# Optimization experiments

Hardware: AMD Instinct MI355X
Metric: run time of the kernel (lower is better)

The kernel has to match this reference:

```python
import jax, jax.numpy as jnp
import numpy as np

N, E, D = 50000, 800000, 128
LN_EPS = 1e-5


def setup_inputs() -> dict:
    key = jax.random.key(0)
    ks = jax.random.split(key, 6)
    return {
        "x": jax.random.normal(ks[0], (N, D), dtype=jnp.float32),
        "edge_index": jax.random.randint(ks[1], (2, E), 0, N, dtype=jnp.int64),
        "edge_weight": jax.random.uniform(ks[2], (E,), dtype=jnp.float32),
        "lin_w": jax.random.normal(ks[3], (D, D), dtype=jnp.float32) * (1.0 / np.sqrt(D)),
        "lin_b": jax.random.normal(ks[4], (D,), dtype=jnp.float32) * 0.02,
        "ln_gamma": jnp.ones((D,), dtype=jnp.float32),
        "ln_beta": jnp.zeros((D,), dtype=jnp.float32),
    }


def reference(x, edge_index, edge_weight, lin_w, lin_b, ln_gamma, ln_beta):
    n = x.shape[0]
    src, dst = edge_index[0], edge_index[1]
    # degree (by dst), symmetric-ish normalization with +1 smoothing
    deg = jax.ops.segment_sum(jnp.ones(dst.shape, x.dtype), dst, num_segments=n)
    dis = jax.lax.rsqrt(deg + 1.0)  # (N,)
    # gather -> scale -> scatter-add
    scale = (edge_weight * dis[src])[:, None]          # (E,1)
    msg = x[src] * scale                               # (E,D)
    agg = jax.ops.segment_sum(msg, dst, num_segments=n)  # (N,D)
    agg = agg * dis[:, None] + x                       # residual
    # dense tail: Linear -> GELU (exact, matches torch F.gelu) -> LayerNorm
    h = jax.nn.gelu(agg @ lin_w.T + lin_b, approximate=False)
    mu = jnp.mean(h, axis=-1, keepdims=True)
    var = jnp.mean(jnp.square(h - mu), axis=-1, keepdims=True)
    return (h - mu) * jax.lax.rsqrt(var + LN_EPS) * ln_gamma + ln_beta
```

## Files before the change

kernel.cpp:

```cpp
#include <hip/hip_runtime.h>
#include <hip/hip_fp16.h>
#include <math.h>

#define D 128
#define CAP 48
#define LDS_STRIDE 136
#define CHUNKS 256
#define BLDS 4096

typedef __bf16  bf16x8 __attribute__((ext_vector_type(8)));
typedef float   f32x4  __attribute__((ext_vector_type(4)));

static __device__ __forceinline__ unsigned short f2bf(float f) {
    unsigned int u = __float_as_uint(f);
    u = (u + 0x7fffu + ((u >> 16) & 1u)) >> 16;
    return (unsigned short)u;
}
static __device__ __forceinline__ unsigned int pack2bf(float lo, float hi) {
    return (unsigned int)f2bf(lo) | ((unsigned int)f2bf(hi) << 16);
}
static __device__ __forceinline__ float bflo(unsigned int u) { return __uint_as_float(u << 16); }
static __device__ __forceinline__ float bfhi(unsigned int u) { return __uint_as_float(u & 0xffff0000u); }


__global__ __launch_bounds__(256) void k_hist(const int* __restrict__ dst,
                                              int* __restrict__ H,
                                              int e_count, int cs, int nbk) {
    __shared__ int hist[1024];
    int tid = threadIdx.x, c = blockIdx.x;
    for (int b = tid; b < nbk; b += 256) hist[b] = 0;
    __syncthreads();
    int lo = c * cs, hi = min(lo + cs, e_count);
    for (int i = lo + tid; i < hi; i += 256) atomicAdd(&hist[dst[i] >> 6], 1);
    __syncthreads();
    for (int b = tid; b < nbk; b += 256) H[b * CHUNKS + c] = hist[b];
}

__global__ __launch_bounds__(256) void k_bsum(const int* __restrict__ a,
                                              int* __restrict__ bsum, int n) {
    int g = blockIdx.x * 256 + threadIdx.x;
    int lane = threadIdx.x & 63, wave = threadIdx.x >> 6;
    int v = (g < n) ? a[g] : 0;
    #pragma unroll
    for (int off = 32; off > 0; off >>= 1) v += __shfl_down(v, off);
    __shared__ int ws[4];
    if (lane == 0) ws[wave] = v;
    __syncthreads();
    if (threadIdx.x == 0) bsum[blockIdx.x] = ws[0] + ws[1] + ws[2] + ws[3];
}

__global__ __launch_bounds__(1024) void k_scan_bsum2(int* __restrict__ bsum, int nb) {
    int tid = threadIdx.x, lane = tid & 63, wave = tid >> 6;
    int v = (tid < nb) ? bsum[tid] : 0;
    int incl = v;
    #pragma unroll
    for (int off = 1; off < 64; off <<= 1) {
        int t = __shfl_up(incl, off);
        if (lane >= off) incl += t;
    }
    __shared__ int ws[16];
    if (lane == 63) ws[wave] = incl;
    __syncthreads();
    if (tid == 0) {
        int run = 0;
        #pragma unroll
        for (int i = 0; i < 16; ++i) { int t = ws[i]; ws[i] = run; run += t; }
    }
    __syncthreads();
    if (tid < nb) bsum[tid] = incl - v + ws[wave];
}

__global__ __launch_bounds__(256) void k_applyH(int* __restrict__ H,
                                                const int* __restrict__ bsum_excl, int m) {
    int g = blockIdx.x * 256 + threadIdx.x;
    int tid = threadIdx.x, lane = tid & 63, wave = tid >> 6;
    int v = (g < m) ? H[g] : 0;
    int incl = v;
    #pragma unroll
    for (int off = 1; off < 64; off <<= 1) {
        int t = __shfl_up(incl, off);
        if (lane >= off) incl += t;
    }
    __shared__ int ws[4];
    if (lane == 63) ws[wave] = incl;
    __syncthreads();
    int add = bsum_excl[blockIdx.x];
    for (int i = 0; i < wave; ++i) add += ws[i];
    if (g < m) H[g] = incl - v + add;
}

__global__ __launch_bounds__(256) void k_scatter(const int* __restrict__ src,
                                                 const int* __restrict__ dst,
                                                 const float* __restrict__ ew,
                                                 const int* __restrict__ H,
                                                 unsigned int* __restrict__ rec,
                                                 int e_count, int cs, int nbk) {
    __shared__ int cur[1024];
    int tid = threadIdx.x, c = blockIdx.x;
    for (int b = tid; b < nbk; b += 256) cur[b] = H[b * CHUNKS + c];
    __syncthreads();
    int lo = c * cs, hi = min(lo + cs, e_count);
    for (int i = lo + tid; i < hi; i += 256) {
        int d = dst[i];
        int s = src[i];
        unsigned int q = (unsigned int)(ew[i] * 1023.0f + 0.5f);
        unsigned int r = (q << 22) | ((unsigned int)(d & 63) << 16) | (unsigned int)s;
        int pos = atomicAdd(&cur[d >> 6], 1);
        rec[pos] = r;
    }
}

__global__ __launch_bounds__(256) void k_bucket_sort(unsigned int* __restrict__ rec,
                                                     const int* __restrict__ H,
                                                     int* __restrict__ deg,
                                                     int* __restrict__ offs,
                                                     int e_count, int n, int nbk) {
    __shared__ int hist[64], curs[64];
    __shared__ unsigned int srt[BLDS];
    int tid = threadIdx.x, b = blockIdx.x;
    int start = H[b * CHUNKS];
    int end = (b == nbk - 1) ? e_count : H[(b + 1) * CHUNKS];
    int cnt = min(end - start, BLDS);
    if (tid < 64) hist[tid] = 0;
    __syncthreads();
    for (int i = tid; i < cnt; i += 256) atomicAdd(&hist[(rec[start + i] >> 16) & 63], 1);
    __syncthreads();
    if (tid < 64) {
        int dg = hist[tid];
        int incl = dg;
        #pragma unroll
        for (int off = 1; off < 64; off <<= 1) {
            int t = __shfl_up(incl, off);
            if (tid >= off) incl += t;
        }
        int excl = incl - dg;
        curs[tid] = excl;
        int node = b * 64 + tid;
        if (node < n) {
            deg[node] = dg;
            offs[node] = start + excl;
            if (node == n - 1) offs[n] = e_count;
        }
    }
    __syncthreads();
    for (int i = tid; i < cnt; i += 256) {
        unsigned int r = rec[start + i];
        int rank = atomicAdd(&curs[(r >> 16) & 63], 1);
        srt[rank] = r;
    }
    __syncthreads();
    for (int i = tid; i < cnt; i += 256) rec[start + i] = srt[i];
}


__global__ __launch_bounds__(256) void k_cast(const float* __restrict__ x,
                                              const int* __restrict__ deg,
                                              unsigned short* __restrict__ xs, int n) {
    int i4 = blockIdx.x * 256 + threadIdx.x;
    int nq = n * (D / 4);
    if (i4 >= nq) return;
    int node = i4 >> 5;
    float dd = rsqrtf((float)deg[node] + 1.0f);
    float4 v = ((const float4*)x)[i4];
    ushort4 u;
    u.x = f2bf(v.x * dd); u.y = f2bf(v.y * dd);
    u.z = f2bf(v.z * dd); u.w = f2bf(v.w * dd);
    ((ushort4*)xs)[i4] = u;
}


__global__ __launch_bounds__(256) void k_gather_csr(const unsigned short* __restrict__ xs,
                                                    const float* __restrict__ x,
                                                    const int* __restrict__ offs,
                                                    const unsigned int* __restrict__ rec,
                                                    unsigned short* __restrict__ aggbf, int n) {
    int node = (int)((blockIdx.x * blockDim.x + threadIdx.x) >> 6);
    int lane = threadIdx.x & 63;
    if (node >= n) return;
    int beg = offs[node], end = offs[node + 1];
    const float wq = 1.0f / 1023.0f;
    float ax = 0.f, ay = 0.f;

    int e = beg;
    for (; e + 3 < end; e += 4) {
        unsigned int r0 = rec[e + 0], r1 = rec[e + 1], r2 = rec[e + 2], r3 = rec[e + 3];
        unsigned int u0 = ((const unsigned int*)(xs + (size_t)(r0 & 0xffffu) * D))[lane];
        unsigned int u1 = ((const unsigned int*)(xs + (size_t)(r1 & 0xffffu) * D))[lane];
        unsigned int u2 = ((const unsigned int*)(xs + (size_t)(r2 & 0xffffu) * D))[lane];
        unsigned int u3 = ((const unsigned int*)(xs + (size_t)(r3 & 0xffffu) * D))[lane];
        float w0 = (float)(r0 >> 22) * wq;
        float w1 = (float)(r1 >> 22) * wq;
        float w2 = (float)(r2 >> 22) * wq;
        float w3 = (float)(r3 >> 22) * wq;
        ax += w0 * bflo(u0); ay += w0 * bfhi(u0);
        ax += w1 * bflo(u1); ay += w1 * bfhi(u1);
        ax += w2 * bflo(u2); ay += w2 * bfhi(u2);
        ax += w3 * bflo(u3); ay += w3 * bfhi(u3);
    }
    for (; e < end; ++e) {
        unsigned int r = rec[e];
        unsigned int u = ((const unsigned int*)(xs + (size_t)(r & 0xffffu) * D))[lane];
        float w = (float)(r >> 22) * wq;
        ax += w * bflo(u); ay += w * bfhi(u);
    }

    float dd = rsqrtf((float)(end - beg) + 1.0f);
    float2 xv = ((const float2*)(x + (size_t)node * D))[lane];
    ((unsigned int*)(aggbf + (size_t)node * D))[lane] = pack2bf(ax * dd + xv.x, ay * dd + xv.y);
}


__global__ __launch_bounds__(256) void k_tail_bf(const unsigned short* __restrict__ aggbf,
                                                 float* __restrict__ out,
                                                 const float* __restrict__ W,
                                                 const float* __restrict__ bias,
                                                 const float* __restrict__ gamma,
                                                 const float* __restrict__ beta, int n) {
    __shared__ unsigned short Bl[128 * LDS_STRIDE];

    int tid  = threadIdx.x;
    int lane = tid & 63;
    int wave = tid >> 6;
    int n16  = lane & 15;
    int quad = lane >> 4;

    #pragma unroll
    for (int it = 0; it < 16; ++it) {
        int idx4 = it * 256 + tid;
        float4 w4 = ((const float4*)W)[idx4];
        int t  = idx4 >> 5;
        int k4 = (idx4 & 31) << 2;
        ushort4 u;
        u.x = f2bf(w4.x); u.y = f2bf(w4.y); u.z = f2bf(w4.z); u.w = f2bf(w4.w);
        *(ushort4*)&Bl[t * LDS_STRIDE + k4] = u;
    }
    __syncthreads();

    int row0w = blockIdx.x * 64 + wave * 16;
    int arow  = row0w + n16;

    bf16x8 afr[4];
    #pragma unroll
    for (int ko = 0; ko < 4; ++ko)
        afr[ko] = __builtin_bit_cast(bf16x8,
            *(const uint4*)&aggbf[(size_t)arow * D + ko * 32 + quad * 8]);

    f32x4 acc[8];
    #pragma unroll
    for (int nt = 0; nt < 8; ++nt) acc[nt] = (f32x4){0.f, 0.f, 0.f, 0.f};

    #pragma unroll
    for (int nt = 0; nt < 8; ++nt) {
        #pragma unroll
        for (int ko = 0; ko < 4; ++ko) {
            bf16x8 bfr = __builtin_bit_cast(bf16x8,
                *(const uint4*)&Bl[(nt * 16 + n16) * LDS_STRIDE + ko * 32 + quad * 8]);
            acc[nt] = __builtin_amdgcn_mfma_f32_16x16x32_bf16(afr[ko], bfr, acc[nt], 0, 0, 0);
        }
    }

    float bcol[8], gcol[8], betcol[8];
    #pragma unroll
    for (int nt = 0; nt < 8; ++nt) {
        int col = nt * 16 + n16;
        bcol[nt]   = bias[col];
        gcol[nt]   = gamma[col];
        betcol[nt] = beta[col];
    }

    #pragma unroll
    for (int r = 0; r < 4; ++r) {
        float h[8];
        float s1 = 0.f, s2 = 0.f;
        #pragma unroll
        for (int nt = 0; nt < 8; ++nt) {
            float v = acc[nt][r] + bcol[nt];
            v = 0.5f * v * (1.0f + erff(v * 0.70710678118654752f));
            h[nt] = v;
            s1 += v; s2 += v * v;
        }
        #pragma unroll
        for (int mask = 1; mask < 16; mask <<= 1) {
            s1 += __shfl_xor(s1, mask);
            s2 += __shfl_xor(s2, mask);
        }
        float mu  = s1 * (1.0f / 128.0f);
        float var = s2 * (1.0f / 128.0f) - mu * mu;
        float inv = rsqrtf(var + 1e-5f);
        int row = row0w + quad * 4 + r;
        if (row < n) {
            #pragma unroll
            for (int nt = 0; nt < 8; ++nt)
                out[(size_t)row * D + nt * 16 + n16] = (h[nt] - mu) * inv * gcol[nt] + betcol[nt];
        }
    }
}


__global__ __launch_bounds__(256) void k_fillp8(const int* __restrict__ src,
                                                const int* __restrict__ dst,
                                                const float* __restrict__ ew,
                                                int* __restrict__ cnt,
                                                int2* __restrict__ rec, int e_count) {
    int e = blockIdx.x * blockDim.x + threadIdx.x;
    if (e >= e_count) return;
    int d = dst[e];
    int pos = atomicAdd(&cnt[d], 1);
    if (pos < CAP)
        rec[(size_t)d * CAP + pos] = make_int2(src[e], __float_as_int(ew[e]));
}

__global__ __launch_bounds__(256) void k_gatherp_f32(const float* __restrict__ x,
                                                     const int* __restrict__ cnt,
                                                     const int2* __restrict__ rec,
                                                     float* __restrict__ agg, int n) {
    int node = (int)((blockIdx.x * blockDim.x + threadIdx.x) >> 6);
    int lane = threadIdx.x & 63;
    if (node >= n) return;
    int c = cnt[node];
    int m = min(c, CAP);
    size_t base = (size_t)node * CAP;
    float ax = 0.f, ay = 0.f;
    for (int i = 0; i < m; ++i) {
        int2 p = rec[base + i];
        float w = __int_as_float(p.y) * rsqrtf((float)cnt[p.x] + 1.0f);
        float2 v = ((const float2*)(x + (size_t)p.x * D))[lane];
        ax += w * v.x; ay += w * v.y;
    }
    float dd = rsqrtf((float)c + 1.0f);
    float2 xv = ((const float2*)(x + (size_t)node * D))[lane];
    float2 o;
    o.x = ax * dd + xv.x;
    o.y = ay * dd + xv.y;
    ((float2*)(agg + (size_t)node * D))[lane] = o;
}

__global__ __launch_bounds__(256) void k_tail_mfma(float* __restrict__ io,
                                                   const float* __restrict__ W,
                                                   const float* __restrict__ bias,
                                                   const float* __restrict__ gamma,
                                                   const float* __restrict__ beta, int n) {
    __shared__ unsigned short Bl[128 * LDS_STRIDE];
    __shared__ unsigned short Al[4][16 * LDS_STRIDE];

    int tid  = threadIdx.x;
    int lane = tid & 63;
    int wave = tid >> 6;
    int n16  = lane & 15;
    int quad = lane >> 4;

    #pragma unroll
    for (int it = 0; it < 16; ++it) {
        int idx4 = it * 256 + tid;
        float4 w4 = ((const float4*)W)[idx4];
        int t  = idx4 >> 5;
        int k4 = (idx4 & 31) << 2;
        ushort4 u;
        u.x = f2bf(w4.x); u.y = f2bf(w4.y); u.z = f2bf(w4.z); u.w = f2bf(w4.w);
        *(ushort4*)&Bl[t * LDS_STRIDE + k4] = u;
    }
    int row0w = blockIdx.x * 64 + wave * 16;
    #pragma unroll
    for (int j = 0; j < 8; ++j) {
        int idx4 = j * 64 + lane;
        int m  = idx4 >> 5;
        int k4 = (idx4 & 31) << 2;
        int row = row0w + m;
        float4 a4 = make_float4(0.f, 0.f, 0.f, 0.f);
        if (row < n) a4 = ((const float4*)(io + (size_t)row * D))[idx4 & 31];
        ushort4 u;
        u.x = f2bf(a4.x); u.y = f2bf(a4.y); u.z = f2bf(a4.z); u.w = f2bf(a4.w);
        *(ushort4*)&Al[wave][m * LDS_STRIDE + k4] = u;
    }
    __syncthreads();

    bf16x8 afr[4];
    #pragma unroll
    for (int ko = 0; ko < 4; ++ko)
        afr[ko] = __builtin_bit_cast(bf16x8,
            *(const uint4*)&Al[wave][n16 * LDS_STRIDE + ko * 32 + quad * 8]);

    f32x4 acc[8];
    #pragma unroll
    for (int nt = 0; nt < 8; ++nt) acc[nt] = (f32x4){0.f, 0.f, 0.f, 0.f};

    #pragma unroll
    for (int nt = 0; nt < 8; ++nt) {
        #pragma unroll
        for (int ko = 0; ko < 4; ++ko) {
            bf16x8 bfr = __builtin_bit_cast(bf16x8,
                *(const uint4*)&Bl[(nt * 16 + n16) * LDS_STRIDE + ko * 32 + quad * 8]);
            acc[nt] = __builtin_amdgcn_mfma_f32_16x16x32_bf16(afr[ko], bfr, acc[nt], 0, 0, 0);
        }
    }

    float bcol[8], gcol[8], betcol[8];
    #pragma unroll
    for (int nt = 0; nt < 8; ++nt) {
        int col = nt * 16 + n16;
        bcol[nt]   = bias[col];
        gcol[nt]   = gamma[col];
        betcol[nt] = beta[col];
    }

    #pragma unroll
    for (int r = 0; r < 4; ++r) {
        float h[8];
        float s1 = 0.f, s2 = 0.f;
        #pragma unroll
        for (int nt = 0; nt < 8; ++nt) {
            float v = acc[nt][r] + bcol[nt];
            v = 0.5f * v * (1.0f + erff(v * 0.70710678118654752f));
            h[nt] = v;
            s1 += v; s2 += v * v;
        }
        #pragma unroll
        for (int mask = 1; mask < 16; mask <<= 1) {
            s1 += __shfl_xor(s1, mask);
            s2 += __shfl_xor(s2, mask);
        }
        float mu  = s1 * (1.0f / 128.0f);
        float var = s2 * (1.0f / 128.0f) - mu * mu;
        float inv = rsqrtf(var + 1e-5f);
        int row = row0w + quad * 4 + r;
        if (row < n) {
            #pragma unroll
            for (int nt = 0; nt < 8; ++nt)
                io[(size_t)row * D + nt * 16 + n16] = (h[nt] - mu) * inv * gcol[nt] + betcol[nt];
        }
    }
}


extern "C" void kernel_launch(void* const* d_in, const int* in_sizes, int n_in,
                              void* d_out, int out_size, void* d_ws, size_t ws_size,
                              hipStream_t stream) {
    const float* x    = (const float*)d_in[0];
    const int*   ei   = (const int*)d_in[1];
    const float* ew   = (const float*)d_in[2];
    const float* linw = (const float*)d_in[3];
    const float* linb = (const float*)d_in[4];
    const float* lng  = (const float*)d_in[5];
    const float* lnb  = (const float*)d_in[6];
    float* out = (float*)d_out;

    int n = in_sizes[0] / D;
    int e = in_sizes[1] / 2;
    const int* src = ei;
    const int* dst = ei + e;

    int nbk = (n + 63) / 64;
    int m   = nbk * CHUNKS;
    int cs  = (e + CHUNKS - 1) / CHUNKS;
    int gb  = (n + 3) / 4;
    int tb  = (n + 63) / 64;

    char* wsp = (char*)d_ws;
    size_t off = 0;
    auto alloc = [&](size_t bytes) { char* p = wsp + off; off = (off + bytes + 255) & ~(size_t)255; return p; };
    int*            H     = (int*)alloc((size_t)m * 4);
    int*            bsumH = (int*)alloc((size_t)nbk * 4);
    unsigned int*   rec   = (unsigned int*)alloc((size_t)e * 4);
    int*            deg   = (int*)alloc((size_t)n * 4);
    int*            offs  = (int*)alloc((size_t)(n + 1) * 4);
    unsigned short* xs    = (unsigned short*)alloc((size_t)n * D * 2);
    unsigned short* aggbf = (unsigned short*)alloc(((size_t)n + 64) * D * 2);
    bool big = (off <= ws_size) && (n <= 65535) && (nbk <= 1024);

    if (big) {
        k_hist<<<CHUNKS, 256, 0, stream>>>(dst, H, e, cs, nbk);
        k_bsum<<<nbk, 256, 0, stream>>>(H, bsumH, m);
        k_scan_bsum2<<<1, 1024, 0, stream>>>(bsumH, nbk);
        k_applyH<<<nbk, 256, 0, stream>>>(H, bsumH, m);
        k_scatter<<<CHUNKS, 256, 0, stream>>>(src, dst, ew, H, rec, e, cs, nbk);
        k_bucket_sort<<<nbk, 256, 0, stream>>>(rec, H, deg, offs, e, n, nbk);
        int cb = (n * (D / 4) + 255) / 256;
        k_cast<<<cb, 256, 0, stream>>>(x, deg, xs, n);
        k_gather_csr<<<gb, 256, 0, stream>>>(xs, x, offs, rec, aggbf, n);
        k_tail_bf<<<tb, 256, 0, stream>>>(aggbf, out, linw, linb, lng, lnb, n);
    } else {
        size_t off2 = 0;
        auto alloc2 = [&](size_t bytes) { char* p = wsp + off2; off2 = (off2 + bytes + 255) & ~(size_t)255; return p; };
        int*  cnt2 = (int*)alloc2((size_t)n * 4);
        int2* rec8 = (int2*)alloc2((size_t)n * CAP * 8);
        hipMemsetAsync(cnt2, 0, (size_t)n * 4, stream);
        int eb = (e + 255) / 256;
        k_fillp8<<<eb, 256, 0, stream>>>(src, dst, ew, cnt2, rec8, e);
        k_gatherp_f32<<<gb, 256, 0, stream>>>(x, cnt2, rec8, out, n);
        k_tail_mfma<<<tb, 256, 0, stream>>>(out, linw, linb, lng, lnb, n);
    }
}
```

Measured before the change: 175.3 us.

## Fuse bf16 cast into bucket sort and split gather into column slices

The separate cast kernel is folded into the bucket-sort kernel: each block scales and converts its own 64 node rows to bf16 using the degree histogram it already holds in LDS. This removes a launch and the deg array round-trip. The gather kernel is reworked so that each block handles one 32-column slice of four nodes. Within a wave, four lane groups process different edges in parallel and are reduced with shuffles. This raises the number of independent loads in flight per node, at the cost of four times as many blocks and re-reading the edge records once per slice.

```diff
diff --git a/kernel.cpp b/kernel.cpp
--- a/kernel.cpp
+++ b/kernel.cpp
@@ -110,11 +110,12 @@
     }
 }
 
-__global__ __launch_bounds__(256) void k_bucket_sort(unsigned int* __restrict__ rec,
-                                                     const int* __restrict__ H,
-                                                     int* __restrict__ deg,
-                                                     int* __restrict__ offs,
-                                                     int e_count, int n, int nbk) {
+__global__ __launch_bounds__(256) void k_bucket_sort_cast(unsigned int* __restrict__ rec,
+                                                          const int* __restrict__ H,
+                                                          const float* __restrict__ x,
+                                                          unsigned short* __restrict__ xs,
+                                                          int* __restrict__ offs,
+                                                          int e_count, int n, int nbk) {
     __shared__ int hist[64], curs[64];
     __shared__ unsigned int srt[BLDS];
     int tid = threadIdx.x, b = blockIdx.x;
@@ -137,12 +138,25 @@
         curs[tid] = excl;
         int node = b * 64 + tid;
         if (node < n) {
-            deg[node] = dg;
             offs[node] = start + excl;
             if (node == n - 1) offs[n] = e_count;
         }
     }
     __syncthreads();
+    #pragma unroll
+    for (int j = 0; j < 8; ++j) {
+        int idx = j * 256 + tid;
+        int rl = idx >> 5;
+        int node = b * 64 + rl;
+        if (node < n) {
+            float dd = rsqrtf((float)hist[rl] + 1.0f);
+            float4 v = ((const float4*)x)[(size_t)node * 32 + (idx & 31)];
+            ushort4 u;
+            u.x = f2bf(v.x * dd); u.y = f2bf(v.y * dd);
+            u.z = f2bf(v.z * dd); u.w = f2bf(v.w * dd);
+            ((ushort4*)xs)[(size_t)node * 32 + (idx & 31)] = u;
+        }
+    }
     for (int i = tid; i < cnt; i += 256) {
         unsigned int r = rec[start + i];
         int rank = atomicAdd(&curs[(r >> 16) & 63], 1);
@@ -153,60 +167,51 @@
 }
 
 
-__global__ __launch_bounds__(256) void k_cast(const float* __restrict__ x,
-                                              const int* __restrict__ deg,
-                                              unsigned short* __restrict__ xs, int n) {
-    int i4 = blockIdx.x * 256 + threadIdx.x;
-    int nq = n * (D / 4);
-    if (i4 >= nq) return;
-    int node = i4 >> 5;
-    float dd = rsqrtf((float)deg[node] + 1.0f);
-    float4 v = ((const float4*)x)[i4];
-    ushort4 u;
-    u.x = f2bf(v.x * dd); u.y = f2bf(v.y * dd);
-    u.z = f2bf(v.z * dd); u.w = f2bf(v.w * dd);
-    ((ushort4*)xs)[i4] = u;
-}
-
-
-__global__ __launch_bounds__(256) void k_gather_csr(const unsigned short* __restrict__ xs,
-                                                    const float* __restrict__ x,
-                                                    const int* __restrict__ offs,
-                                                    const unsigned int* __restrict__ rec,
-                                                    unsigned short* __restrict__ aggbf, int n) {
-    int node = (int)((blockIdx.x * blockDim.x + threadIdx.x) >> 6);
+__global__ __launch_bounds__(256) void k_gather_slice(const unsigned short* __restrict__ xs,
+                                                      const float* __restrict__ x,
+                                                      const int* __restrict__ offs,
+                                                      const unsigned int* __restrict__ rec,
+                                                      unsigned short* __restrict__ aggbf, int n) {
+    int slice = blockIdx.x & 3;
+    int wave  = threadIdx.x >> 6;
+    int node  = (blockIdx.x >> 2) * 4 + wave;
+    if (node >= n) return;
     int lane = threadIdx.x & 63;
-    if (node >= n) return;
+    int g    = lane >> 4;
+    int l    = lane & 15;
     int beg = offs[node], end = offs[node + 1];
+    int m = end - beg;
     const float wq = 1.0f / 1023.0f;
+    size_t soff = (size_t)slice * 32 + (size_t)l * 2;
+
     float ax = 0.f, ay = 0.f;
-
-    int e = beg;
-    for (; e + 3 < end; e += 4) {
-        unsigned int r0 = rec[e + 0], r1 = rec[e + 1], r2 = rec[e + 2], r3 = rec[e + 3];
-        unsigned int u0 = ((const unsigned int*)(xs + (size_t)(r0 & 0xffffu) * D))[lane];
-        unsigned int u1 = ((const unsigned int*)(xs + (size_t)(r1 & 0xffffu) * D))[lane];
-        unsigned int u2 = ((const unsigned int*)(xs + (size_t)(r2 & 0xffffu) * D))[lane];
-        unsigned int u3 = ((const unsigned int*)(xs + (size_t)(r3 & 0xffffu) * D))[lane];
+    int i = 0;
+    for (; i + 7 < m; i += 8) {
+        unsigned int r0 = rec[beg + i + g];
+        unsigned int r1 = rec[beg + i + 4 + g];
+        unsigned int u0 = *(const unsigned int*)(xs + (size_t)(r0 & 0xffffu) * D + soff);
+        unsigned int u1 = *(const unsigned int*)(xs + (size_t)(r1 & 0xffffu) * D + soff);
         float w0 = (float)(r0 >> 22) * wq;
         float w1 = (float)(r1 >> 22) * wq;
-        float w2 = (float)(r2 >> 22) * wq;
-        float w3 = (float)(r3 >> 22) * wq;
         ax += w0 * bflo(u0); ay += w0 * bfhi(u0);
         ax += w1 * bflo(u1); ay += w1 * bfhi(u1);
-        ax += w2 * bflo(u2); ay += w2 * bfhi(u2);
-        ax += w3 * bflo(u3); ay += w3 * bfhi(u3);
-    }
-    for (; e < end; ++e) {
-        unsigned int r = rec[e];
-        unsigned int u = ((const unsigned int*)(xs + (size_t)(r & 0xffffu) * D))[lane];
-        float w = (float)(r >> 22) * wq;
-        ax += w * bflo(u); ay += w * bfhi(u);
-    }
-
-    float dd = rsqrtf((float)(end - beg) + 1.0f);
-    float2 xv = ((const float2*)(x + (size_t)node * D))[lane];
-    ((unsigned int*)(aggbf + (size_t)node * D))[lane] = pack2bf(ax * dd + xv.x, ay * dd + xv.y);
+    }
+    for (; i < m; i += 4) {
+        if (i + g < m) {
+            unsigned int r = rec[beg + i + g];
+            unsigned int u = *(const unsigned int*)(xs + (size_t)(r & 0xffffu) * D + soff);
+            float w = (float)(r >> 22) * wq;
+            ax += w * bflo(u); ay += w * bfhi(u);
+        }
+    }
+    ax += __shfl_xor(ax, 16); ay += __shfl_xor(ay, 16);
+    ax += __shfl_xor(ax, 32); ay += __shfl_xor(ay, 32);
+
+    if (g == 0) {
+        float dd = rsqrtf((float)m + 1.0f);
+        float2 xv = ((const float2*)(x + (size_t)node * D + slice * 32))[l];
+        *(unsigned int*)(aggbf + (size_t)node * D + soff) = pack2bf(ax * dd + xv.x, ay * dd + xv.y);
+    }
 }
 
 
@@ -452,7 +457,6 @@
     int nbk = (n + 63) / 64;
     int m   = nbk * CHUNKS;
     int cs  = (e + CHUNKS - 1) / CHUNKS;
-    int gb  = (n + 3) / 4;
     int tb  = (n + 63) / 64;
 
     char* wsp = (char*)d_ws;
@@ -461,7 +465,6 @@
     int*            H     = (int*)alloc((size_t)m * 4);
     int*            bsumH = (int*)alloc((size_t)nbk * 4);
     unsigned int*   rec   = (unsigned int*)alloc((size_t)e * 4);
-    int*            deg   = (int*)alloc((size_t)n * 4);
     int*            offs  = (int*)alloc((size_t)(n + 1) * 4);
     unsigned short* xs    = (unsigned short*)alloc((size_t)n * D * 2);
     unsigned short* aggbf = (unsigned short*)alloc(((size_t)n + 64) * D * 2);
@@ -473,10 +476,9 @@
         k_scan_bsum2<<<1, 1024, 0, stream>>>(bsumH, nbk);
         k_applyH<<<nbk, 256, 0, stream>>>(H, bsumH, m);
         k_scatter<<<CHUNKS, 256, 0, stream>>>(src, dst, ew, H, rec, e, cs, nbk);
-        k_bucket_sort<<<nbk, 256, 0, stream>>>(rec, H, deg, offs, e, n, nbk);
-        int cb = (n * (D / 4) + 255) / 256;
-        k_cast<<<cb, 256, 0, stream>>>(x, deg, xs, n);
-        k_gather_csr<<<gb, 256, 0, stream>>>(xs, x, offs, rec, aggbf, n);
+        k_bucket_sort_cast<<<nbk, 256, 0, stream>>>(rec, H, x, xs, offs, e, n, nbk);
+        int gsb = ((n + 3) / 4) * 4;
+        k_gather_slice<<<gsb, 256, 0, stream>>>(xs, x, offs, rec, aggbf, n);
         k_tail_bf<<<tb, 256, 0, stream>>>(aggbf, out, linw, linb, lng, lnb, n);
     } else {
         size_t off2 = 0;
@@ -485,6 +487,7 @@
         int2* rec8 = (int2*)alloc2((size_t)n * CAP * 8);
         hipMemsetAsync(cnt2, 0, (size_t)n * 4, stream);
         int eb = (e + 255) / 256;
+        int gb = (n + 3) / 4;
         k_fillp8<<<eb, 256, 0, stream>>>(src, dst, ew, cnt2, rec8, e);
         k_gatherp_f32<<<gb, 256, 0, stream>>>(x, cnt2, rec8, out, n);
         k_tail_mfma<<<tb, 256, 0, stream>>>(out, linw, linb, lng, lnb, n);
```

Result: slower. 221.8 us (+26.5%).
